# Kernel optimization log

Measured on AMD Instinct MI355X. Metric: run time of the kernel, lower is better.

## Reference

```python
import jax, jax.numpy as jnp
import numpy as np

N, P, D, FDIM, TFEAT = 65536, 6, 256, 8, 16
RAW_DIM = 4 + TFEAT  # 20
IN_DIM = 3 + FDIM + 3 + 3  # xyz + frame embedding + rigid xyz + viewdir = 17


def setup_inputs() -> dict:
    key = jax.random.key(0)
    ks = jax.random.split(key, 16)
    inp = {
        "tpts": jax.random.normal(ks[0], (N, P, 3), jnp.float32),
        "bigpts": jax.random.normal(ks[1], (N, P, 3), jnp.float32),
        "viewdir": jax.random.normal(ks[2], (N, P, 3), jnp.float32),
        "dists": jax.random.uniform(ks[3], (N,), jnp.float32),
        "part_dist": jax.random.uniform(ks[4], (1, N, P), jnp.float32),
        "frame_dim": jax.random.normal(ks[5], (FDIM,), jnp.float32),
        "W1": jax.random.normal(ks[6], (P, IN_DIM, D), jnp.float32) / np.sqrt(IN_DIM),
        "b1": jax.random.normal(ks[7], (P, D), jnp.float32) * 0.01,
        "W2": jax.random.normal(ks[8], (P, D, D), jnp.float32) / np.sqrt(D),
        "b2": jax.random.normal(ks[9], (P, D), jnp.float32) * 0.01,
        "W3": jax.random.normal(ks[10], (P, D, RAW_DIM), jnp.float32) / np.sqrt(D),
        "b3": jax.random.normal(ks[11], (P, RAW_DIM), jnp.float32) * 0.01,
        "Wocc": jax.random.normal(ks[12], (P, D, 1), jnp.float32) / np.sqrt(D),
        "bocc": jax.random.normal(ks[13], (P, 1), jnp.float32) * 0.01,
        "tflag": jax.random.randint(ks[14], (N, P), 0, 2).astype(bool),
    }
    return inp


def _part_mlps(tpts, bigpts, viewdir, frame_dim, W1, b1, W2, b2, W3, b3, Wocc, bocc):
    # Run all P part networks on all N points (batched per-part GEMMs).
    n = tpts.shape[0]
    frame = jnp.broadcast_to(frame_dim, (n, P, FDIM))
    x = jnp.concatenate([tpts, frame, bigpts, viewdir], axis=-1)  # (N,P,17)
    h = jax.nn.relu(jnp.einsum('npi,pid->npd', x, W1) + b1)
    h = jax.nn.relu(jnp.einsum('npd,pde->npe', h, W2) + b2)
    raw_p = jnp.einsum('npd,pdr->npr', h, W3) + b3               # (N,P,20)
    occ_p = jax.nn.sigmoid(jnp.einsum('npd,pdo->npo', h, Wocc) + bocc)  # (N,P,1)
    return raw_p, occ_p


def reference(tpts, bigpts, viewdir, dists, part_dist, frame_dim,
              W1, b1, W2, b2, W3, b3, Wocc, bocc, tflag):
    raw_p, occ_p = _part_mlps(tpts, bigpts, viewdir, frame_dim,
                              W1, b1, W2, b2, W3, b3, Wocc, bocc)
    # scatter-back equivalent: unflagged (point, part) slots stay zero
    flag = tflag[..., None].astype(raw_p.dtype)  # (N,P,1)
    raws = raw_p * flag                           # (N,P,20)
    occs = occ_p * flag                           # (N,P,1)
    # cfg.aggr == 'mean'
    raw = raws.mean(axis=1)                       # (N,20)
    occ = occs.mean(axis=1)                       # (N,1)
    tocc = occs[..., 0]                           # (N,P)
    return jnp.concatenate([raw, occ, tocc], axis=-1)  # (N, 20+1+P)
```

## Files before the change

### kernel.cpp

```cpp
#include <hip/hip_runtime.h>
#include <hip/hip_bf16.h>

using bf16 = __hip_bfloat16;
typedef __bf16 bf16x8 __attribute__((ext_vector_type(8)));
typedef __bf16 bf16x4v __attribute__((ext_vector_type(4)));
typedef float f32x4 __attribute__((ext_vector_type(4)));

#define MFMA16(a, b, c) __builtin_amdgcn_mfma_f32_16x16x32_bf16((a), (b), (c), 0, 0, 0)


__global__ void prep_kernel(const float* __restrict__ W1, const float* __restrict__ b1,
                            const float* __restrict__ W2, const float* __restrict__ W3,
                            const float* __restrict__ Wocc, __bf16* __restrict__ ws) {
  const int t = blockIdx.x * 256 + threadIdx.x;
  if (t < 49152) {
    const int p = t >> 13, r = t & 8191, n = r >> 5, c = r & 31;
    const float* src = W2 + p * 65536 + c * 8 * 256 + n;
    bf16x8 v;
#pragma unroll
    for (int j = 0; j < 8; ++j) v[j] = (__bf16)src[j * 256];
    *reinterpret_cast<bf16x8*>(&ws[49152 + p * 65536 + n * 256 + c * 8]) = v;
  } else if (t < 55296) {
    const int u = t - 49152;
    const int p = u >> 10, r = u & 1023, n = r >> 2, c = r & 3;
    bf16x8 v;
#pragma unroll
    for (int j = 0; j < 8; ++j) {
      const int k = c * 8 + j;
      float x = 0.f;
      if (k < 17) {
        const int ko = (k < 8) ? k + 3 : ((k < 11) ? k - 8 : k);
        x = W1[p * 4352 + ko * 256 + n];
      } else if (k == 17) {
        x = b1[p * 256 + n];
      }
      v[j] = (__bf16)x;
    }
    *reinterpret_cast<bf16x8*>(&ws[p * 8192 + n * 32 + c * 8]) = v;
  } else if (t < 61440) {
    const int u = t - 55296;
    const int p = u >> 10, r = u & 1023, row = r >> 5, c = r & 31;
    bf16x8 v;
#pragma unroll
    for (int j = 0; j < 8; ++j) {
      const int k = c * 8 + j;
      float x = 0.f;
      if (row < 20)       x = W3[p * 5120 + k * 20 + row];
      else if (row == 20) x = Wocc[p * 256 + k];
      v[j] = (__bf16)x;
    }
    *reinterpret_cast<bf16x8*>(&ws[442368 + p * 8192 + row * 256 + c * 8]) = v;
  }
}

__global__ __launch_bounds__(256, 2) void tpose_main(
    const float* __restrict__ tpts, const float* __restrict__ bigpts,
    const float* __restrict__ viewdir, const float* __restrict__ frame,
    const float* __restrict__ b2g, const float* __restrict__ b3g,
    const float* __restrict__ boccg, const int* __restrict__ tflag,
    const __bf16* __restrict__ ws, float* __restrict__ out) {
  const __bf16* __restrict__ W1t = ws;
  const __bf16* __restrict__ W2t = ws + 49152;
  const __bf16* __restrict__ W3t = ws + 442368;

  __shared__ __align__(16) __bf16 Xf[128 * 40];
  __shared__ __align__(16) __bf16 Hf[128 * 256];

  const int tid = threadIdx.x;
  const int w = tid >> 6;
  const int lane = tid & 63;
  const int lq = lane >> 4;
  const int ln = lane & 15;
  const int e = ln & 7;
  const int n0 = blockIdx.x * 128;

  if (tid < 128) {
    bf16x8 f8;
#pragma unroll
    for (int j = 0; j < 8; ++j) f8[j] = (__bf16)frame[j];
    *reinterpret_cast<bf16x8*>(&Xf[tid * 40]) = f8;
    bf16x8 z = {};
    z[1] = (__bf16)1.0f;
    *reinterpret_cast<bf16x8*>(&Xf[tid * 40 + 16]) = z;
    bf16x8 z2 = {};
    *reinterpret_cast<bf16x8*>(&Xf[tid * 40 + 24]) = z2;
  }

  const int role = tid & 3;
  const float* __restrict__ dynsrc =
      (role == 0) ? tpts : (role == 1) ? bigpts : viewdir;

  float pre[2][3];
  float flv[2];
#pragma unroll
  for (int pass = 0; pass < 2; ++pass) {
    const int pt = (tid >> 2) + pass * 64;
    const int base3 = (n0 + pt) * 18;
#pragma unroll
    for (int i = 0; i < 3; ++i) pre[pass][i] = dynsrc[base3 + i];
  }
#pragma unroll
  for (int s = 0; s < 2; ++s)
    flv[s] = (tflag[(n0 + w * 32 + s * 16 + ln) * 6] != 0) ? 1.f : 0.f;

  float psum0[2][4] = {{0.f, 0.f, 0.f, 0.f}, {0.f, 0.f, 0.f, 0.f}};
  float psum1[2][4] = {{0.f, 0.f, 0.f, 0.f}, {0.f, 0.f, 0.f, 0.f}};

  for (int p = 0; p < 6; ++p) {
    if (role < 3) {
#pragma unroll
      for (int pass = 0; pass < 2; ++pass) {
        const int pt = (tid >> 2) + pass * 64;
#pragma unroll
        for (int i = 0; i < 3; ++i)
          Xf[pt * 40 + 8 + role * 3 + i] = (__bf16)pre[pass][i];
      }
    }

    const int pn = (p < 5) ? p + 1 : 5;
    float fln[2];
#pragma unroll
    for (int pass = 0; pass < 2; ++pass) {
      const int pt = (tid >> 2) + pass * 64;
      const int base3 = ((n0 + pt) * 6 + pn) * 3;
#pragma unroll
      for (int i = 0; i < 3; ++i) pre[pass][i] = dynsrc[base3 + i];
    }
#pragma unroll
    for (int s = 0; s < 2; ++s)
      fln[s] = (tflag[(n0 + w * 32 + s * 16 + ln) * 6 + pn] != 0) ? 1.f : 0.f;

    bf16x8 aw[4];
#pragma unroll
    for (int mt = 0; mt < 4; ++mt)
      aw[mt] = *reinterpret_cast<const bf16x8*>(
          &W1t[p * 8192 + (w * 64 + mt * 16 + ln) * 32 + lq * 8]);

    __syncthreads();

    f32x4 acc[4][8];
#pragma unroll
    for (int mt = 0; mt < 4; ++mt)
#pragma unroll
      for (int nt = 0; nt < 8; ++nt) acc[mt][nt] = f32x4{0.f, 0.f, 0.f, 0.f};
#pragma unroll
    for (int nt = 0; nt < 8; ++nt) {
      const bf16x8 xb =
          *reinterpret_cast<const bf16x8*>(&Xf[(nt * 16 + ln) * 40 + lq * 8]);
#pragma unroll
      for (int mt = 0; mt < 4; ++mt) acc[mt][nt] = MFMA16(aw[mt], xb, acc[mt][nt]);
    }
#pragma unroll
    for (int mt = 0; mt < 4; ++mt) {
      const int c = w * 8 + mt * 2 + (lq >> 1);
      const int off = ((c ^ e) << 3) + (lq & 1) * 4;
#pragma unroll
      for (int nt = 0; nt < 8; ++nt) {
        bf16x4v hv;
#pragma unroll
        for (int r = 0; r < 4; ++r) hv[r] = (__bf16)fmaxf(acc[mt][nt][r], 0.f);
        *reinterpret_cast<bf16x4v*>(&Hf[(nt * 16 + ln) * 256 + off]) = hv;
      }
    }

    __syncthreads();

    {
      f32x4 b2v[4];
#pragma unroll
      for (int mt = 0; mt < 4; ++mt)
        b2v[mt] = *reinterpret_cast<const f32x4*>(
            &b2g[p * 256 + w * 64 + mt * 16 + lq * 4]);
#pragma unroll
      for (int mt = 0; mt < 4; ++mt)
#pragma unroll
        for (int nt = 0; nt < 8; ++nt) acc[mt][nt] = b2v[mt];
    }
    const __bf16* __restrict__ w2p = W2t + p * 65536 + (w * 64 + ln) * 256 + lq * 8;
    {
      bf16x8 a2[4];
#pragma unroll
      for (int mt = 0; mt < 4; ++mt)
        a2[mt] = *reinterpret_cast<const bf16x8*>(w2p + mt * 4096);
#pragma unroll
      for (int kk = 0; kk < 8; ++kk) {
        bf16x8 a2n[4];
        if (kk < 7) {
#pragma unroll
          for (int mt = 0; mt < 4; ++mt)
            a2n[mt] = *reinterpret_cast<const bf16x8*>(
                w2p + mt * 4096 + (kk + 1) * 32);
        }
#pragma unroll
        for (int nt = 0; nt < 8; ++nt) {
          const bf16x8 hb = *reinterpret_cast<const bf16x8*>(
              &Hf[(nt * 16 + ln) * 256 + (((kk * 4 + lq) ^ e) << 3)]);
#pragma unroll
          for (int mt = 0; mt < 4; ++mt) acc[mt][nt] = MFMA16(a2[mt], hb, acc[mt][nt]);
        }
#pragma unroll
        for (int mt = 0; mt < 4; ++mt) a2[mt] = a2n[mt];
      }
    }

    __syncthreads();

#pragma unroll
    for (int mt = 0; mt < 4; ++mt) {
      const int c = w * 8 + mt * 2 + (lq >> 1);
      const int off = ((c ^ e) << 3) + (lq & 1) * 4;
#pragma unroll
      for (int nt = 0; nt < 8; ++nt) {
        bf16x4v hv;
#pragma unroll
        for (int r = 0; r < 4; ++r) hv[r] = (__bf16)fmaxf(acc[mt][nt][r], 0.f);
        *reinterpret_cast<bf16x4v*>(&Hf[(nt * 16 + ln) * 256 + off]) = hv;
      }
    }

    __syncthreads();

    f32x4 acc3[2][2];
    {
      float b3v[2][4];
#pragma unroll
      for (int mt = 0; mt < 2; ++mt)
#pragma unroll
        for (int r = 0; r < 4; ++r) {
          const int d = mt * 16 + lq * 4 + r;
          float v = 0.f;
          if (d < 20)       v = b3g[p * 20 + d];
          else if (d == 20) v = boccg[p];
          b3v[mt][r] = v;
        }
#pragma unroll
      for (int mt = 0; mt < 2; ++mt)
#pragma unroll
        for (int s = 0; s < 2; ++s)
#pragma unroll
          for (int r = 0; r < 4; ++r) acc3[mt][s][r] = b3v[mt][r];
    }
    const __bf16* __restrict__ w3p = W3t + p * 8192 + ln * 256 + lq * 8;
#pragma unroll
    for (int kk = 0; kk < 8; ++kk) {
      bf16x8 a3[2];
#pragma unroll
      for (int mt = 0; mt < 2; ++mt)
        a3[mt] = *reinterpret_cast<const bf16x8*>(w3p + mt * 4096 + kk * 32);
#pragma unroll
      for (int s = 0; s < 2; ++s) {
        const bf16x8 hb = *reinterpret_cast<const bf16x8*>(
            &Hf[(w * 32 + s * 16 + ln) * 256 + (((kk * 4 + lq) ^ e) << 3)]);
#pragma unroll
        for (int mt = 0; mt < 2; ++mt) acc3[mt][s] = MFMA16(a3[mt], hb, acc3[mt][s]);
      }
    }

#pragma unroll
    for (int s = 0; s < 2; ++s) {
      const int pt = n0 + w * 32 + s * 16 + ln;
#pragma unroll
      for (int r = 0; r < 4; ++r) psum0[s][r] += flv[s] * acc3[0][s][r];
      if (lq == 0) {
#pragma unroll
        for (int r = 0; r < 4; ++r) psum1[s][r] += flv[s] * acc3[1][s][r];
      } else if (lq == 1) {
        const float occ = 1.f / (1.f + __expf(-acc3[1][s][0]));
        out[pt * 27 + 21 + p] = flv[s] * occ;
        psum1[s][0] += flv[s] * occ;
      }
    }

    flv[0] = fln[0];
    flv[1] = fln[1];
  }

  const float inv6 = 1.f / 6.f;
#pragma unroll
  for (int s = 0; s < 2; ++s) {
    const int pt = n0 + w * 32 + s * 16 + ln;
#pragma unroll
    for (int r = 0; r < 4; ++r) out[pt * 27 + lq * 4 + r] = psum0[s][r] * inv6;
    if (lq == 0) {
#pragma unroll
      for (int r = 0; r < 4; ++r) out[pt * 27 + 16 + r] = psum1[s][r] * inv6;
    } else if (lq == 1) {
      out[pt * 27 + 20] = psum1[s][0] * inv6;
    }
  }
}

extern "C" void kernel_launch(void* const* d_in, const int* in_sizes, int n_in,
                              void* d_out, int out_size, void* d_ws, size_t ws_size,
                              hipStream_t stream) {
  const float* tpts    = (const float*)d_in[0];
  const float* bigpts  = (const float*)d_in[1];
  const float* viewdir = (const float*)d_in[2];
  const float* frame   = (const float*)d_in[5];
  const float* W1      = (const float*)d_in[6];
  const float* b1      = (const float*)d_in[7];
  const float* W2      = (const float*)d_in[8];
  const float* b2      = (const float*)d_in[9];
  const float* W3      = (const float*)d_in[10];
  const float* b3      = (const float*)d_in[11];
  const float* Wocc    = (const float*)d_in[12];
  const float* bocc    = (const float*)d_in[13];
  const int*   tflag   = (const int*)d_in[14];
  __bf16* ws  = (__bf16*)d_ws;
  float*  out = (float*)d_out;

  prep_kernel<<<240, 256, 0, stream>>>(W1, b1, W2, W3, Wocc, ws);
  tpose_main<<<512, 256, 0, stream>>>(tpts, bigpts, viewdir, frame, b2, b3,
                                      bocc, tflag, ws, out);
}
```

Measured before the change: 199.1 us.

## Tile W2 transpose via shared memory, stage output coalesced, reorder prefetch

The W2 transpose in the prep kernel now goes through a padded shared-memory tile, so global reads are coalesced instead of strided, and the launch uses fewer blocks. The main kernel collects the per-part occupancies and the final outputs in shared memory. It then writes each 128-point output block with contiguous 16-byte stores instead of scattered 4-byte stores. The W2 and bias loads are hoisted ahead of the next-part input prefetch to reorder latency. The cost is extra LDS for Tocc and an extra barrier at the end.

```diff
diff --git a/kernel.cpp b/kernel.cpp
--- a/kernel.cpp
+++ b/kernel.cpp
@@ -12,15 +12,31 @@
 __global__ void prep_kernel(const float* __restrict__ W1, const float* __restrict__ b1,
                             const float* __restrict__ W2, const float* __restrict__ W3,
                             const float* __restrict__ Wocc, __bf16* __restrict__ ws) {
-  const int t = blockIdx.x * 256 + threadIdx.x;
-  if (t < 49152) {
-    const int p = t >> 13, r = t & 8191, n = r >> 5, c = r & 31;
-    const float* src = W2 + p * 65536 + c * 8 * 256 + n;
-    bf16x8 v;
-#pragma unroll
-    for (int j = 0; j < 8; ++j) v[j] = (__bf16)src[j * 256];
-    *reinterpret_cast<bf16x8*>(&ws[49152 + p * 65536 + n * 256 + c * 8]) = v;
-  } else if (t < 55296) {
+  const int b = blockIdx.x;
+  const int tid = threadIdx.x;
+  if (b < 96) {
+    __shared__ float tile[64][65];
+    const int p = b >> 4, t = b & 15;
+    const int d0 = (t >> 2) * 64, e0 = (t & 3) * 64;
+    const int lane = tid & 63, grp = tid >> 6;
+    const float* src = W2 + p * 65536 + (d0 + grp * 16) * 256 + e0 + lane;
+#pragma unroll
+    for (int i = 0; i < 16; ++i) tile[grp * 16 + i][lane] = src[i * 256];
+    __syncthreads();
+#pragma unroll
+    for (int q = 0; q < 2; ++q) {
+      const int m = tid + q * 256;
+      const int ee = m >> 3, c = m & 7;
+      bf16x8 v;
+#pragma unroll
+      for (int j = 0; j < 8; ++j) v[j] = (__bf16)tile[c * 8 + j][ee];
+      *reinterpret_cast<bf16x8*>(
+          &ws[49152 + p * 65536 + (e0 + ee) * 256 + d0 + c * 8]) = v;
+    }
+    return;
+  }
+  const int t = 49152 + (b - 96) * 256 + tid;
+  if (t < 55296) {
     const int u = t - 49152;
     const int p = u >> 10, r = u & 1023, n = r >> 2, c = r & 3;
     bf16x8 v;
@@ -65,6 +81,7 @@
 
   __shared__ __align__(16) __bf16 Xf[128 * 40];
   __shared__ __align__(16) __bf16 Hf[128 * 256];
+  __shared__ float Tocc[128 * 6];
 
   const int tid = threadIdx.x;
   const int w = tid >> 6;
@@ -117,6 +134,52 @@
       }
     }
 
+    bf16x8 aw[4];
+#pragma unroll
+    for (int mt = 0; mt < 4; ++mt)
+      aw[mt] = *reinterpret_cast<const bf16x8*>(
+          &W1t[p * 8192 + (w * 64 + mt * 16 + ln) * 32 + lq * 8]);
+
+    __syncthreads();
+
+    f32x4 acc[4][8];
+#pragma unroll
+    for (int mt = 0; mt < 4; ++mt)
+#pragma unroll
+      for (int nt = 0; nt < 8; ++nt) acc[mt][nt] = f32x4{0.f, 0.f, 0.f, 0.f};
+#pragma unroll
+    for (int nt = 0; nt < 8; ++nt) {
+      const bf16x8 xb =
+          *reinterpret_cast<const bf16x8*>(&Xf[(nt * 16 + ln) * 40 + lq * 8]);
+#pragma unroll
+      for (int mt = 0; mt < 4; ++mt) acc[mt][nt] = MFMA16(aw[mt], xb, acc[mt][nt]);
+    }
+#pragma unroll
+    for (int mt = 0; mt < 4; ++mt) {
+      const int c = w * 8 + mt * 2 + (lq >> 1);
+      const int off = ((c ^ e) << 3) + (lq & 1) * 4;
+#pragma unroll
+      for (int nt = 0; nt < 8; ++nt) {
+        bf16x4v hv;
+#pragma unroll
+        for (int r = 0; r < 4; ++r) hv[r] = (__bf16)fmaxf(acc[mt][nt][r], 0.f);
+        *reinterpret_cast<bf16x4v*>(&Hf[(nt * 16 + ln) * 256 + off]) = hv;
+      }
+    }
+
+    __syncthreads();
+
+    const __bf16* __restrict__ w2p = W2t + p * 65536 + (w * 64 + ln) * 256 + lq * 8;
+    bf16x8 a2[4];
+#pragma unroll
+    for (int mt = 0; mt < 4; ++mt)
+      a2[mt] = *reinterpret_cast<const bf16x8*>(w2p + mt * 4096);
+    f32x4 b2v[4];
+#pragma unroll
+    for (int mt = 0; mt < 4; ++mt)
+      b2v[mt] = *reinterpret_cast<const f32x4*>(
+          &b2g[p * 256 + w * 64 + mt * 16 + lq * 4]);
+
     const int pn = (p < 5) ? p + 1 : 5;
     float fln[2];
 #pragma unroll
@@ -130,58 +193,11 @@
     for (int s = 0; s < 2; ++s)
       fln[s] = (tflag[(n0 + w * 32 + s * 16 + ln) * 6 + pn] != 0) ? 1.f : 0.f;
 
-    bf16x8 aw[4];
-#pragma unroll
-    for (int mt = 0; mt < 4; ++mt)
-      aw[mt] = *reinterpret_cast<const bf16x8*>(
-          &W1t[p * 8192 + (w * 64 + mt * 16 + ln) * 32 + lq * 8]);
-
-    __syncthreads();
-
-    f32x4 acc[4][8];
-#pragma unroll
-    for (int mt = 0; mt < 4; ++mt)
-#pragma unroll
-      for (int nt = 0; nt < 8; ++nt) acc[mt][nt] = f32x4{0.f, 0.f, 0.f, 0.f};
-#pragma unroll
-    for (int nt = 0; nt < 8; ++nt) {
-      const bf16x8 xb =
-          *reinterpret_cast<const bf16x8*>(&Xf[(nt * 16 + ln) * 40 + lq * 8]);
-#pragma unroll
-      for (int mt = 0; mt < 4; ++mt) acc[mt][nt] = MFMA16(aw[mt], xb, acc[mt][nt]);
-    }
-#pragma unroll
-    for (int mt = 0; mt < 4; ++mt) {
-      const int c = w * 8 + mt * 2 + (lq >> 1);
-      const int off = ((c ^ e) << 3) + (lq & 1) * 4;
-#pragma unroll
-      for (int nt = 0; nt < 8; ++nt) {
-        bf16x4v hv;
-#pragma unroll
-        for (int r = 0; r < 4; ++r) hv[r] = (__bf16)fmaxf(acc[mt][nt][r], 0.f);
-        *reinterpret_cast<bf16x4v*>(&Hf[(nt * 16 + ln) * 256 + off]) = hv;
-      }
-    }
-
-    __syncthreads();
-
+#pragma unroll
+    for (int mt = 0; mt < 4; ++mt)
+#pragma unroll
+      for (int nt = 0; nt < 8; ++nt) acc[mt][nt] = b2v[mt];
     {
-      f32x4 b2v[4];
-#pragma unroll
-      for (int mt = 0; mt < 4; ++mt)
-        b2v[mt] = *reinterpret_cast<const f32x4*>(
-            &b2g[p * 256 + w * 64 + mt * 16 + lq * 4]);
-#pragma unroll
-      for (int mt = 0; mt < 4; ++mt)
-#pragma unroll
-        for (int nt = 0; nt < 8; ++nt) acc[mt][nt] = b2v[mt];
-    }
-    const __bf16* __restrict__ w2p = W2t + p * 65536 + (w * 64 + ln) * 256 + lq * 8;
-    {
-      bf16x8 a2[4];
-#pragma unroll
-      for (int mt = 0; mt < 4; ++mt)
-        a2[mt] = *reinterpret_cast<const bf16x8*>(w2p + mt * 4096);
 #pragma unroll
       for (int kk = 0; kk < 8; ++kk) {
         bf16x8 a2n[4];
@@ -258,7 +274,6 @@
 
 #pragma unroll
     for (int s = 0; s < 2; ++s) {
-      const int pt = n0 + w * 32 + s * 16 + ln;
 #pragma unroll
       for (int r = 0; r < 4; ++r) psum0[s][r] += flv[s] * acc3[0][s][r];
       if (lq == 0) {
@@ -266,7 +281,7 @@
         for (int r = 0; r < 4; ++r) psum1[s][r] += flv[s] * acc3[1][s][r];
       } else if (lq == 1) {
         const float occ = 1.f / (1.f + __expf(-acc3[1][s][0]));
-        out[pt * 27 + 21 + p] = flv[s] * occ;
+        Tocc[(w * 32 + s * 16 + ln) * 6 + p] = flv[s] * occ;
         psum1[s][0] += flv[s] * occ;
       }
     }
@@ -275,18 +290,33 @@
     flv[1] = fln[1];
   }
 
+  __syncthreads();
+  float* stage = reinterpret_cast<float*>(Hf);
   const float inv6 = 1.f / 6.f;
 #pragma unroll
   for (int s = 0; s < 2; ++s) {
-    const int pt = n0 + w * 32 + s * 16 + ln;
-#pragma unroll
-    for (int r = 0; r < 4; ++r) out[pt * 27 + lq * 4 + r] = psum0[s][r] * inv6;
+    const int ptl = w * 32 + s * 16 + ln;
+#pragma unroll
+    for (int r = 0; r < 4; ++r) stage[ptl * 27 + lq * 4 + r] = psum0[s][r] * inv6;
     if (lq == 0) {
 #pragma unroll
-      for (int r = 0; r < 4; ++r) out[pt * 27 + 16 + r] = psum1[s][r] * inv6;
+      for (int r = 0; r < 4; ++r) stage[ptl * 27 + 16 + r] = psum1[s][r] * inv6;
     } else if (lq == 1) {
-      out[pt * 27 + 20] = psum1[s][0] * inv6;
-    }
+      stage[ptl * 27 + 20] = psum1[s][0] * inv6;
+    }
+  }
+  if (tid < 128) {
+#pragma unroll
+    for (int pp = 0; pp < 6; ++pp) stage[tid * 27 + 21 + pp] = Tocc[tid * 6 + pp];
+  }
+  __syncthreads();
+  float* outp = out + (size_t)n0 * 27;
+#pragma unroll
+  for (int q = 0; q < 4; ++q) {
+    const int m = tid + q * 256;
+    if (m < 864)
+      *reinterpret_cast<f32x4*>(&outp[m * 4]) =
+          *reinterpret_cast<const f32x4*>(&stage[m * 4]);
   }
 }
 
@@ -309,7 +339,7 @@
   __bf16* ws  = (__bf16*)d_ws;
   float*  out = (float*)d_out;
 
-  prep_kernel<<<240, 256, 0, stream>>>(W1, b1, W2, W3, Wocc, ws);
+  prep_kernel<<<144, 256, 0, stream>>>(W1, b1, W2, W3, Wocc, ws);
   tpose_main<<<512, 256, 0, stream>>>(tpts, bigpts, viewdir, frame, b2, b3,
                                       bocc, tflag, ws, out);
 }
```

New measurement: 192.4 us. -3.4%, faster.
